# Kernel tuning notes

Measured on AMD Instinct MI355X. Metric: run time of the kernel, lower is better.

Reference implementation:

```python
import jax, jax.numpy as jnp
import numpy as np
from jax import lax

B = 32768
IMG = 28  # MNIST image side
K = 3     # conv kernel side
OUT_HW = IMG - K + 1  # 26 -> 676 flattened


def setup_inputs() -> dict:
    key = jax.random.key(0)
    ks = jax.random.split(key, 6)
    return {
        "x": jax.random.normal(ks[0], (B, IMG * IMG), dtype=jnp.float32),
        "conv_w": jax.random.normal(ks[1], (K, K), dtype=jnp.float32),
        "w0": jax.random.normal(ks[2], (200, OUT_HW * OUT_HW), dtype=jnp.float32) * 0.04,
        "b0": jax.random.normal(ks[3], (200,), dtype=jnp.float32) * 0.01,
        "w1": jax.random.normal(ks[4], (10, 200), dtype=jnp.float32) * 0.07,
        "b1": jax.random.normal(ks[5], (10,), dtype=jnp.float32) * 0.01,
    }


def reference(x, conv_w, w0, b0, w1, b1):
    # Valid 2D cross-correlation (matches the torch tensordot patch loop)
    xi = x.reshape(-1, 1, IMG, IMG)              # [B,1,28,28]
    kern = conv_w[None, None, :, :]              # [1,1,3,3]
    y = lax.conv_general_dilated(
        xi, kern, window_strides=(1, 1), padding="VALID",
        dimension_numbers=("NCHW", "OIHW", "NCHW"))  # [B,1,26,26]
    flat = y.reshape(y.shape[0], OUT_HW * OUT_HW)    # [B,676]
    h = jax.nn.relu(flat @ w0.T + b0)                # [B,200]
    return h @ w1.T + b1                             # [B,10] logits
```

## Files before the change

### kernel.cpp

```cpp
#include <hip/hip_runtime.h>
#include <hip/hip_bf16.h>

#define IMG 28
#define OHW 26
#define NPIX 676
#define KT_N 22
#define NT_N 13
#define NH 200
#define NOUT 10
#define MT 32
#define ASTRIDE 712
#define HSTRIDE 208

typedef __attribute__((ext_vector_type(8))) short bf16x8;
typedef __attribute__((ext_vector_type(4))) float f32x4;

static __device__ __forceinline__ unsigned short bf16_bits(float v) {
    __hip_bfloat16 b = __float2bfloat16(v);
    return *(unsigned short*)&b;
}

__global__ void pack_weights(const float* __restrict__ w0,
                             __hip_bfloat16* __restrict__ Bf) {
    int idx = blockIdx.x * blockDim.x + threadIdx.x;
    if (idx >= NT_N * KT_N * 512) return;
    int j = idx & 7, L = (idx >> 3) & 63, kt = (idx >> 9) % KT_N, nt = idx / (KT_N * 512);
    int n = nt * 16 + (L & 15), k = kt * 32 + ((L >> 4) << 3) + j;
    float v = (n < NH && k < NPIX) ? w0[n * NPIX + k] : 0.f;
    Bf[idx] = __float2bfloat16(v);
}

__global__ __launch_bounds__(512, 6) void fused_mlp_kernel(
    const float* __restrict__ x,
    const float* __restrict__ cw,
    const __hip_bfloat16* __restrict__ Bf,
    const float* __restrict__ b0,
    const float* __restrict__ w1,
    const float* __restrict__ b1,
    float* __restrict__ out)
{
    __shared__ __align__(16) char lds_raw[MT * ASTRIDE * 2];
    __hip_bfloat16* A = (__hip_bfloat16*)lds_raw;
    float* H = (float*)lds_raw;

    const int tid = threadIdx.x;
    const int img0 = blockIdx.x * MT;

    const float k00 = cw[0], k01 = cw[1], k02 = cw[2];
    const float k10 = cw[3], k11 = cw[4], k12 = cw[5];
    const float k20 = cw[6], k21 = cw[7], k22 = cw[8];

    for (int idx = tid; idx < MT * (ASTRIDE - NPIX); idx += 512) {
        int i = idx / (ASTRIDE - NPIX);
        int c = idx - i * (ASTRIDE - NPIX);
        ((unsigned short*)A)[i * ASTRIDE + NPIX + c] = 0;
    }

    for (int task = tid; task < MT * OHW; task += 512) {
        int img  = task / OHW;
        int orow = task - img * OHW;
        const float* base = x + (size_t)(img0 + img) * (IMG * IMG) + orow * IMG;

        float4 r0[7], r1[7], r2[7];
#pragma unroll
        for (int j = 0; j < 7; ++j) {
            r0[j] = ((const float4*)base)[j];
            r1[j] = ((const float4*)(base + IMG))[j];
            r2[j] = ((const float4*)(base + 2 * IMG))[j];
        }
        const float* a0r = (const float*)r0;
        const float* a1r = (const float*)r1;
        const float* a2r = (const float*)r2;

        unsigned short obits[OHW];
#pragma unroll
        for (int c = 0; c < OHW; ++c) {
            float acc = a0r[c] * k00 + a0r[c + 1] * k01 + a0r[c + 2] * k02
                      + a1r[c] * k10 + a1r[c + 1] * k11 + a1r[c + 2] * k12
                      + a2r[c] * k20 + a2r[c + 1] * k21 + a2r[c + 2] * k22;
            obits[c] = bf16_bits(acc);
        }
        unsigned* dst = (unsigned*)(A + img * ASTRIDE + orow * OHW);
#pragma unroll
        for (int c2 = 0; c2 < 13; ++c2) {
            dst[c2] = (unsigned)obits[2 * c2] | ((unsigned)obits[2 * c2 + 1] << 16);
        }
    }
    __syncthreads();

    const int wave = tid >> 6;
    const int lane = tid & 63;
    const int lm   = lane & 15;
    const int q    = lane >> 4;
    const int ntbase = (wave < 5) ? wave * 2 : 10 + (wave - 5);
    const int ntn    = (wave < 5) ? 2 : 1;

    f32x4 acc[2][2];
#pragma unroll
    for (int m = 0; m < 2; ++m)
#pragma unroll
        for (int t = 0; t < 2; ++t) acc[m][t] = (f32x4){0.f, 0.f, 0.f, 0.f};

    {
        const __hip_bfloat16* a0 = A + lm * ASTRIDE + q * 8;
        const __hip_bfloat16* a1 = A + (16 + lm) * ASTRIDE + q * 8;
        const bf16x8* bb = (const bf16x8*)Bf + (size_t)ntbase * KT_N * 64 + lane;

        if (ntn == 2) {
            for (int kt = 0; kt < KT_N; ++kt) {
                bf16x8 af0 = *(const bf16x8*)(a0 + kt * 32);
                bf16x8 af1 = *(const bf16x8*)(a1 + kt * 32);
                bf16x8 bf0 = bb[kt * 64];
                bf16x8 bf1 = bb[(KT_N + kt) * 64];
                acc[0][0] = __builtin_amdgcn_mfma_f32_16x16x32_bf16(af0, bf0, acc[0][0], 0, 0, 0);
                acc[1][0] = __builtin_amdgcn_mfma_f32_16x16x32_bf16(af1, bf0, acc[1][0], 0, 0, 0);
                acc[0][1] = __builtin_amdgcn_mfma_f32_16x16x32_bf16(af0, bf1, acc[0][1], 0, 0, 0);
                acc[1][1] = __builtin_amdgcn_mfma_f32_16x16x32_bf16(af1, bf1, acc[1][1], 0, 0, 0);
            }
        } else {
            for (int kt = 0; kt < KT_N; ++kt) {
                bf16x8 af0 = *(const bf16x8*)(a0 + kt * 32);
                bf16x8 af1 = *(const bf16x8*)(a1 + kt * 32);
                bf16x8 bf0 = bb[kt * 64];
                acc[0][0] = __builtin_amdgcn_mfma_f32_16x16x32_bf16(af0, bf0, acc[0][0], 0, 0, 0);
                acc[1][0] = __builtin_amdgcn_mfma_f32_16x16x32_bf16(af1, bf0, acc[1][0], 0, 0, 0);
            }
        }
    }
    __syncthreads();

#pragma unroll
    for (int t = 0; t < 2; ++t) {
        if (t < ntn) {
            int n = (ntbase + t) * 16 + lm;
            if (n < NH) {
                float bv = b0[n];
#pragma unroll
                for (int m = 0; m < 2; ++m) {
#pragma unroll
                    for (int r = 0; r < 4; ++r) {
                        int mm = m * 16 + q * 4 + r;
                        float v = acc[m][t][r] + bv;
                        H[mm * HSTRIDE + n] = v > 0.f ? v : 0.f;
                    }
                }
            }
        }
    }
    __syncthreads();

    if (tid < MT * NOUT) {
        int i = tid / NOUT;
        int j = tid - i * NOUT;
        const float4* hrow = (const float4*)(H + i * HSTRIDE);
        const float4* wrow = (const float4*)(w1 + j * NH);
        float s = b1[j];
        float4 accv = {0.f, 0.f, 0.f, 0.f};
#pragma unroll 10
        for (int n = 0; n < NH / 4; ++n) {
            float4 h4 = hrow[n];
            float4 w4 = wrow[n];
            accv.x += h4.x * w4.x;
            accv.y += h4.y * w4.y;
            accv.z += h4.z * w4.z;
            accv.w += h4.w * w4.w;
        }
        s += (accv.x + accv.y) + (accv.z + accv.w);
        out[(size_t)(img0 + i) * NOUT + j] = s;
    }
}

extern "C" void kernel_launch(void* const* d_in, const int* in_sizes, int n_in,
                              void* d_out, int out_size, void* d_ws, size_t ws_size,
                              hipStream_t stream) {
    const float* x   = (const float*)d_in[0];
    const float* cw  = (const float*)d_in[1];
    const float* w0  = (const float*)d_in[2];
    const float* b0  = (const float*)d_in[3];
    const float* w1  = (const float*)d_in[4];
    const float* b1  = (const float*)d_in[5];
    float* out = (float*)d_out;

    __hip_bfloat16* Bf = (__hip_bfloat16*)d_ws;

    const int pack_elems = NT_N * KT_N * 512;
    pack_weights<<<(pack_elems + 255) / 256, 256, 0, stream>>>(w0, Bf);

    fused_mlp_kernel<<<32768 / MT, 512, 0, stream>>>(x, cw, Bf, b0, w1, b1, out);
}
```

Before: 202.0 us.

## Stage input images through LDS slabs for coalesced loads in convolution

Each wave now loads one whole image into a per-wave LDS slab with coalesced float4 loads. It then computes the 3x3 convolution two output pixels per lane, reading the slab. Before, each thread loaded three full rows straight from global memory with strided per-thread access. The change adds 25.6KB of LDS and eight block-wide barriers, and lowers the launch-bounds occupancy hint from 6 to 4.

```diff
diff --git a/kernel.cpp b/kernel.cpp
--- a/kernel.cpp
+++ b/kernel.cpp
@@ -11,6 +11,7 @@
 #define MT 32
 #define ASTRIDE 712
 #define HSTRIDE 208
+#define SLAB 800
 
 typedef __attribute__((ext_vector_type(8))) short bf16x8;
 typedef __attribute__((ext_vector_type(4))) float f32x4;
@@ -30,7 +31,7 @@
     Bf[idx] = __float2bfloat16(v);
 }
 
-__global__ __launch_bounds__(512, 6) void fused_mlp_kernel(
+__global__ __launch_bounds__(512, 4) void fused_mlp_kernel(
     const float* __restrict__ x,
     const float* __restrict__ cw,
     const __hip_bfloat16* __restrict__ Bf,
@@ -40,10 +41,13 @@
     float* __restrict__ out)
 {
     __shared__ __align__(16) char lds_raw[MT * ASTRIDE * 2];
+    __shared__ __align__(16) float simg[8][SLAB];
     __hip_bfloat16* A = (__hip_bfloat16*)lds_raw;
     float* H = (float*)lds_raw;
 
-    const int tid = threadIdx.x;
+    const int tid  = threadIdx.x;
+    const int wave = tid >> 6;
+    const int L    = tid & 63;
     const int img0 = blockIdx.x * MT;
 
     const float k00 = cw[0], k01 = cw[1], k02 = cw[2];
@@ -56,42 +60,44 @@
         ((unsigned short*)A)[i * ASTRIDE + NPIX + c] = 0;
     }
 
-    for (int task = tid; task < MT * OHW; task += 512) {
-        int img  = task / OHW;
-        int orow = task - img * OHW;
-        const float* base = x + (size_t)(img0 + img) * (IMG * IMG) + orow * IMG;
+    for (int p = 0; p < 4; ++p) {
+        const int imgl = p * 8 + wave;
+        const float4* src = (const float4*)(x + (size_t)(img0 + imgl) * (IMG * IMG));
+        float4* slab4 = (float4*)simg[wave];
+        slab4[L]       = src[L];
+        slab4[L + 64]  = src[L + 64];
+        slab4[L + 128] = src[L + 128];
+        if (L < 4) slab4[L + 192] = src[L + 192];
+        __syncthreads();
 
-        float4 r0[7], r1[7], r2[7];
+        const float* buf = simg[wave];
+        unsigned short* abase = (unsigned short*)A + imgl * ASTRIDE;
 #pragma unroll
-        for (int j = 0; j < 7; ++j) {
-            r0[j] = ((const float4*)base)[j];
-            r1[j] = ((const float4*)(base + IMG))[j];
-            r2[j] = ((const float4*)(base + 2 * IMG))[j];
+        for (int t = 0; t < 6; ++t) {
+            int pp = L + (t << 6);
+            if (pp < 338) {
+                int p2 = pp * 2;
+                int r  = p2 / OHW;
+                int c  = p2 - r * OHW;
+                const float* bp = buf + r * IMG + c;
+                float2 r0a = *(const float2*)(bp),           r0b = *(const float2*)(bp + 2);
+                float2 r1a = *(const float2*)(bp + IMG),     r1b = *(const float2*)(bp + IMG + 2);
+                float2 r2a = *(const float2*)(bp + 2 * IMG), r2b = *(const float2*)(bp + 2 * IMG + 2);
+                float o0 = r0a.x * k00 + r0a.y * k01 + r0b.x * k02
+                         + r1a.x * k10 + r1a.y * k11 + r1b.x * k12
+                         + r2a.x * k20 + r2a.y * k21 + r2b.x * k22;
+                float o1 = r0a.y * k00 + r0b.x * k01 + r0b.y * k02
+                         + r1a.y * k10 + r1b.x * k11 + r1b.y * k12
+                         + r2a.y * k20 + r2b.x * k21 + r2b.y * k22;
+                unsigned u = (unsigned)bf16_bits(o0) | ((unsigned)bf16_bits(o1) << 16);
+                *(unsigned*)(abase + p2) = u;
+            }
         }
-        const float* a0r = (const float*)r0;
-        const float* a1r = (const float*)r1;
-        const float* a2r = (const float*)r2;
+        __syncthreads();
+    }
 
-        unsigned short obits[OHW];
-#pragma unroll
-        for (int c = 0; c < OHW; ++c) {
-            float acc = a0r[c] * k00 + a0r[c + 1] * k01 + a0r[c + 2] * k02
-                      + a1r[c] * k10 + a1r[c + 1] * k11 + a1r[c + 2] * k12
-                      + a2r[c] * k20 + a2r[c + 1] * k21 + a2r[c + 2] * k22;
-            obits[c] = bf16_bits(acc);
-        }
-        unsigned* dst = (unsigned*)(A + img * ASTRIDE + orow * OHW);
-#pragma unroll
-        for (int c2 = 0; c2 < 13; ++c2) {
-            dst[c2] = (unsigned)obits[2 * c2] | ((unsigned)obits[2 * c2 + 1] << 16);
-        }
-    }
-    __syncthreads();
-
-    const int wave = tid >> 6;
-    const int lane = tid & 63;
-    const int lm   = lane & 15;
-    const int q    = lane >> 4;
+    const int lm = L & 15;
+    const int q  = L >> 4;
     const int ntbase = (wave < 5) ? wave * 2 : 10 + (wave - 5);
     const int ntn    = (wave < 5) ? 2 : 1;
 
@@ -104,7 +110,7 @@
     {
         const __hip_bfloat16* a0 = A + lm * ASTRIDE + q * 8;
         const __hip_bfloat16* a1 = A + (16 + lm) * ASTRIDE + q * 8;
-        const bf16x8* bb = (const bf16x8*)Bf + (size_t)ntbase * KT_N * 64 + lane;
+        const bf16x8* bb = (const bf16x8*)Bf + (size_t)ntbase * KT_N * 64 + L;
 
         if (ntn == 2) {
             for (int kt = 0; kt < KT_N; ++kt) {
```

After: 190.5 us. -5.7%, faster.

## Fold conv into first-layer weights and run GEMM directly on raw pixels

Applied to the files above, without the earlier changes.

Because the convolution and the first linear layer are both linear, the 3x3 kernel is folded into w0 to build an effective 200x784 weight matrix, packed as bf16 in MFMA layout. The main kernel no longer computes the convolution; it converts the raw 784 input pixels to bf16 with coalesced float4 loads into LDS and runs a K=800 GEMM. That replaces per-row conv arithmetic and strided loads at the cost of about 16% more MFMA K-steps. The GEMM loop also software-prefetches the next B fragment from global memory. Rounding now happens on raw x and on the folded weights rather than on the conv output, which changes the numerics slightly.

```diff
diff --git a/kernel.cpp b/kernel.cpp
--- a/kernel.cpp
+++ b/kernel.cpp
@@ -2,96 +2,121 @@
 #include <hip/hip_bf16.h>
 
 #define IMG 28
-#define OHW 26
-#define NPIX 676
-#define KT_N 22
-#define NT_N 13
+#define KX 784
+#define KT 25
+#define NT 13
 #define NH 200
 #define NOUT 10
 #define MT 32
-#define ASTRIDE 712
+#define AS 808
 #define HSTRIDE 208
 
 typedef __attribute__((ext_vector_type(8))) short bf16x8;
 typedef __attribute__((ext_vector_type(4))) float f32x4;
+typedef __attribute__((ext_vector_type(4))) short s16x4;
 
 static __device__ __forceinline__ unsigned short bf16_bits(float v) {
     __hip_bfloat16 b = __float2bfloat16(v);
     return *(unsigned short*)&b;
 }
 
-__global__ void pack_weights(const float* __restrict__ w0,
-                             __hip_bfloat16* __restrict__ Bf) {
+__global__ void build_weff(const float* __restrict__ w0, const float* __restrict__ cw,
+                           __hip_bfloat16* __restrict__ Bf) {
     int idx = blockIdx.x * blockDim.x + threadIdx.x;
-    if (idx >= NT_N * KT_N * 512) return;
-    int j = idx & 7, L = (idx >> 3) & 63, kt = (idx >> 9) % KT_N, nt = idx / (KT_N * 512);
-    int n = nt * 16 + (L & 15), k = kt * 32 + ((L >> 4) << 3) + j;
-    float v = (n < NH && k < NPIX) ? w0[n * NPIX + k] : 0.f;
-    Bf[idx] = __float2bfloat16(v);
+    if (idx >= NT * KT * 512) return;
+    int j = idx & 7, L = (idx >> 3) & 63, kt = (idx >> 9) % KT, nt = idx / (KT * 512);
+    int n = nt * 16 + (L & 15);
+    int k = kt * 32 + ((L >> 4) << 3) + j;
+    float acc = 0.f;
+    if (n < NH && k < KX) {
+        int u = k / IMG, v = k - u * IMG;
+#pragma unroll
+        for (int i = 0; i < 3; ++i) {
+#pragma unroll
+            for (int jj = 0; jj < 3; ++jj) {
+                int r = u - i, c = v - jj;
+                if (r >= 0 && r < 26 && c >= 0 && c < 26)
+                    acc += cw[i * 3 + jj] * w0[n * 676 + r * 26 + c];
+            }
+        }
+    }
+    Bf[idx] = __float2bfloat16(acc);
 }
 
-__global__ __launch_bounds__(512, 6) void fused_mlp_kernel(
+template <int NTN>
+static __device__ __forceinline__ void gemm_loop(
+    const __hip_bfloat16* __restrict__ a0p, const __hip_bfloat16* __restrict__ a1p,
+    const bf16x8* __restrict__ bb, f32x4 acc[2][2])
+{
+    bf16x8 bc0 = bb[0];
+    bf16x8 bc1 = (NTN == 2) ? bb[KT * 64] : bc0;
+    for (int kt = 0; kt < KT; ++kt) {
+        bf16x8 bn0 = bc0, bn1 = bc1;
+        if (kt < KT - 1) {
+            bn0 = bb[(kt + 1) * 64];
+            if (NTN == 2) bn1 = bb[(KT + kt + 1) * 64];
+        }
+        bf16x8 af0 = *(const bf16x8*)(a0p + kt * 32);
+        bf16x8 af1 = *(const bf16x8*)(a1p + kt * 32);
+        acc[0][0] = __builtin_amdgcn_mfma_f32_16x16x32_bf16(af0, bc0, acc[0][0], 0, 0, 0);
+        acc[1][0] = __builtin_amdgcn_mfma_f32_16x16x32_bf16(af1, bc0, acc[1][0], 0, 0, 0);
+        if (NTN == 2) {
+            acc[0][1] = __builtin_amdgcn_mfma_f32_16x16x32_bf16(af0, bc1, acc[0][1], 0, 0, 0);
+            acc[1][1] = __builtin_amdgcn_mfma_f32_16x16x32_bf16(af1, bc1, acc[1][1], 0, 0, 0);
+        }
+        bc0 = bn0; bc1 = bn1;
+    }
+}
+
+__global__ __launch_bounds__(512, 6) void gemm_fused_kernel(
     const float* __restrict__ x,
-    const float* __restrict__ cw,
     const __hip_bfloat16* __restrict__ Bf,
     const float* __restrict__ b0,
     const float* __restrict__ w1,
     const float* __restrict__ b1,
     float* __restrict__ out)
 {
-    __shared__ __align__(16) char lds_raw[MT * ASTRIDE * 2];
+    __shared__ __align__(16) char lds_raw[MT * AS * 2];
     __hip_bfloat16* A = (__hip_bfloat16*)lds_raw;
     float* H = (float*)lds_raw;
 
-    const int tid = threadIdx.x;
+    const int tid  = threadIdx.x;
+    const int wave = tid >> 6;
+    const int L    = tid & 63;
+    const int lm   = L & 15;
+    const int q    = L >> 4;
     const int img0 = blockIdx.x * MT;
 
-    const float k00 = cw[0], k01 = cw[1], k02 = cw[2];
-    const float k10 = cw[3], k11 = cw[4], k12 = cw[5];
-    const float k20 = cw[6], k21 = cw[7], k22 = cw[8];
-
-    for (int idx = tid; idx < MT * (ASTRIDE - NPIX); idx += 512) {
-        int i = idx / (ASTRIDE - NPIX);
-        int c = idx - i * (ASTRIDE - NPIX);
-        ((unsigned short*)A)[i * ASTRIDE + NPIX + c] = 0;
+    {
+        int row = tid >> 4, c = KX + (tid & 15);
+        ((unsigned short*)A)[row * AS + c] = 0;
     }
 
-    for (int task = tid; task < MT * OHW; task += 512) {
-        int img  = task / OHW;
-        int orow = task - img * OHW;
-        const float* base = x + (size_t)(img0 + img) * (IMG * IMG) + orow * IMG;
-
-        float4 r0[7], r1[7], r2[7];
+    {
+        const float4* xx = (const float4*)(x + (size_t)img0 * KX);
+        float4 v[13];
 #pragma unroll
-        for (int j = 0; j < 7; ++j) {
-            r0[j] = ((const float4*)base)[j];
-            r1[j] = ((const float4*)(base + IMG))[j];
-            r2[j] = ((const float4*)(base + 2 * IMG))[j];
+        for (int t = 0; t < 13; ++t) {
+            int f = tid + 512 * t;
+            v[t] = (f < MT * 196) ? xx[f] : (float4){0.f, 0.f, 0.f, 0.f};
         }
-        const float* a0r = (const float*)r0;
-        const float* a1r = (const float*)r1;
-        const float* a2r = (const float*)r2;
-
-        unsigned short obits[OHW];
 #pragma unroll
-        for (int c = 0; c < OHW; ++c) {
-            float acc = a0r[c] * k00 + a0r[c + 1] * k01 + a0r[c + 2] * k02
-                      + a1r[c] * k10 + a1r[c + 1] * k11 + a1r[c + 2] * k12
-                      + a2r[c] * k20 + a2r[c + 1] * k21 + a2r[c + 2] * k22;
-            obits[c] = bf16_bits(acc);
-        }
-        unsigned* dst = (unsigned*)(A + img * ASTRIDE + orow * OHW);
-#pragma unroll
-        for (int c2 = 0; c2 < 13; ++c2) {
-            dst[c2] = (unsigned)obits[2 * c2] | ((unsigned)obits[2 * c2 + 1] << 16);
+        for (int t = 0; t < 13; ++t) {
+            int f = tid + 512 * t;
+            if (f < MT * 196) {
+                int row  = f / 196;
+                int col4 = f - row * 196;
+                s16x4 p;
+                p.x = (short)bf16_bits(v[t].x);
+                p.y = (short)bf16_bits(v[t].y);
+                p.z = (short)bf16_bits(v[t].z);
+                p.w = (short)bf16_bits(v[t].w);
+                *(s16x4*)(A + row * AS + col4 * 4) = p;
+            }
         }
     }
     __syncthreads();
 
-    const int wave = tid >> 6;
-    const int lane = tid & 63;
-    const int lm   = lane & 15;
-    const int q    = lane >> 4;
     const int ntbase = (wave < 5) ? wave * 2 : 10 + (wave - 5);
     const int ntn    = (wave < 5) ? 2 : 1;
 
@@ -102,30 +127,11 @@
         for (int t = 0; t < 2; ++t) acc[m][t] = (f32x4){0.f, 0.f, 0.f, 0.f};
 
     {
-        const __hip_bfloat16* a0 = A + lm * ASTRIDE + q * 8;
-        const __hip_bfloat16* a1 = A + (16 + lm) * ASTRIDE + q * 8;
-        const bf16x8* bb = (const bf16x8*)Bf + (size_t)ntbase * KT_N * 64 + lane;
-
-        if (ntn == 2) {
-            for (int kt = 0; kt < KT_N; ++kt) {
-                bf16x8 af0 = *(const bf16x8*)(a0 + kt * 32);
-                bf16x8 af1 = *(const bf16x8*)(a1 + kt * 32);
-                bf16x8 bf0 = bb[kt * 64];
-                bf16x8 bf1 = bb[(KT_N + kt) * 64];
-                acc[0][0] = __builtin_amdgcn_mfma_f32_16x16x32_bf16(af0, bf0, acc[0][0], 0, 0, 0);
-                acc[1][0] = __builtin_amdgcn_mfma_f32_16x16x32_bf16(af1, bf0, acc[1][0], 0, 0, 0);
-                acc[0][1] = __builtin_amdgcn_mfma_f32_16x16x32_bf16(af0, bf1, acc[0][1], 0, 0, 0);
-                acc[1][1] = __builtin_amdgcn_mfma_f32_16x16x32_bf16(af1, bf1, acc[1][1], 0, 0, 0);
-            }
-        } else {
-            for (int kt = 0; kt < KT_N; ++kt) {
-                bf16x8 af0 = *(const bf16x8*)(a0 + kt * 32);
-                bf16x8 af1 = *(const bf16x8*)(a1 + kt * 32);
-                bf16x8 bf0 = bb[kt * 64];
-                acc[0][0] = __builtin_amdgcn_mfma_f32_16x16x32_bf16(af0, bf0, acc[0][0], 0, 0, 0);
-                acc[1][0] = __builtin_amdgcn_mfma_f32_16x16x32_bf16(af1, bf0, acc[1][0], 0, 0, 0);
-            }
-        }
+        const __hip_bfloat16* a0p = A + lm * AS + q * 8;
+        const __hip_bfloat16* a1p = A + (16 + lm) * AS + q * 8;
+        const bf16x8* bb = (const bf16x8*)Bf + (size_t)ntbase * KT * 64 + L;
+        if (ntn == 2) gemm_loop<2>(a0p, a1p, bb, acc);
+        else          gemm_loop<1>(a0p, a1p, bb, acc);
     }
     __syncthreads();
 
@@ -183,8 +189,8 @@
 
     __hip_bfloat16* Bf = (__hip_bfloat16*)d_ws;
 
-    const int pack_elems = NT_N * KT_N * 512;
-    pack_weights<<<(pack_elems + 255) / 256, 256, 0, stream>>>(w0, Bf);
+    const int pack_elems = NT * KT * 512;
+    build_weff<<<(pack_elems + 255) / 256, 256, 0, stream>>>(w0, cw, Bf);
 
-    fused_mlp_kernel<<<32768 / MT, 512, 0, stream>>>(x, cw, Bf, b0, w1, b1, out);
+    gemm_fused_kernel<<<32768 / MT, 512, 0, stream>>>(x, Bf, b0, w1, b1, out);
 }
```

Result: faster. 187.4 us (-7.2%).
